# Kernel optimization log

Hardware: AMD Instinct MI355X
Metric: run time of the kernel (lower is better)

Reference implementation:

```python
import jax, jax.numpy as jnp
import numpy as np

K = -1.0          # manifold curvature (hyperbolic / Poincare ball)
SK = 1.0          # sqrt(|K|)
EPS = 1e-7


def _artan_k(x):
    # inverse of tan_k for K<0: artanh(sqrt(|K|) x)/sqrt(|K|)
    return jnp.arctanh(jnp.clip(SK * x, -1.0 + EPS, 1.0 - EPS)) / SK


def _tan_k(x):
    return jnp.tanh(SK * x) / SK


def _norm(x):
    return jnp.maximum(jnp.linalg.norm(x, axis=-1, keepdims=True), 1e-15)


def mobius_add(x, y):
    xy = jnp.sum(x * y, -1, keepdims=True)
    x2 = jnp.sum(x * x, -1, keepdims=True)
    y2 = jnp.sum(y * y, -1, keepdims=True)
    num = (1.0 - 2.0 * K * xy - K * y2) * x + (1.0 + K * x2) * y
    den = 1.0 - 2.0 * K * xy + K * K * x2 * y2
    return num / jnp.maximum(den, 1e-15)


def mobius_scalar_mul(r, x):
    # r may be scalar or (n,1) per-row scalar
    xn = _norm(x)
    return _tan_k(r * _artan_k(xn)) * x / xn


def mobius_matvec(W, x):
    # geoopt convention: (m @ x) per point -> x @ W^T
    xn = _norm(x)
    mx = x @ W.T
    mxn = _norm(mx)
    return _tan_k(mxn / xn * _artan_k(xn)) * mx / mxn


def lambda_x(x):
    # conformal factor lambda_x = 2 / (1 + K |x|^2); returns shape (...,)
    return 2.0 / jnp.maximum(1.0 + K * jnp.sum(x * x, -1), 1e-10)


def expmap0(u):
    un = _norm(u)
    return _tan_k(un) * u / un


def logmap0(y):
    yn = _norm(y)
    return _artan_k(yn) * y / yn


def kappa_left_multiply(A, X):
    # Vectorized per-node weighted gyro-midpoint + mobius scalar mul.
    # out_i = (sum_j A_ij) otimes gyromidpoint(X, weights=A_i)
    gamma = lambda_x(X)                              # (n,)
    denom = A @ (gamma - 1.0)                        # (n,)
    denom = jnp.where(jnp.abs(denom) < 1e-10, 1e-10, denom)
    nom = A @ (gamma[:, None] * X)                   # (n,d)
    two_mean = nom / denom[:, None]
    m = mobius_scalar_mul(0.5, two_mean)             # gyromidpoint
    return mobius_scalar_mul(jnp.sum(A, axis=1, keepdims=True), m)


def setup_inputs() -> dict:
    key = jax.random.key(0)
    k1, k2, k3, k4, k5 = jax.random.split(key, 5)
    n, d, c = 8192, 256, 16
    # node embeddings on the Poincare ball (small norm, well inside the ball)
    X = 0.01 * jax.random.normal(k1, (n, d), jnp.float32)
    # dense normalized adjacency (positive weights, row sums O(1))
    A_hat = jax.random.uniform(k2, (n, n), dtype=jnp.float32) / n
    W = jax.random.uniform(k3, (d, d), dtype=jnp.float32)        # torch.rand init
    W_logits = jax.random.uniform(k4, (d, c), dtype=jnp.float32)
    # p_ks = expmap0(rand), scaled for numerical stability
    p_ks = expmap0(0.05 * jax.random.uniform(k5, (c, d), dtype=jnp.float32))
    return {"X": X, "A_hat": A_hat, "W": W, "W_logits": W_logits, "p_ks": p_ks}


def reference(X, A_hat, W, W_logits, p_ks):
    # hidden kappa-GCN layer
    XW = mobius_matvec(W, X)                          # (n,d)
    AXW = kappa_left_multiply(A_hat, XW)              # (n,d)
    H1 = expmap0(jax.nn.relu(logmap0(AXW)))           # manifold.apply(relu)
    # hyperbolic logits (kappa != 0 branch, K<0 -> asinh)
    z = mobius_add(-p_ks[None, :, :], H1[:, None, :]) # (n,k,d)
    z_n = jnp.linalg.norm(z, axis=-1)                 # (n,k)
    a_n = jnp.maximum(jnp.linalg.norm(W_logits, axis=0), 1e-15)  # (k,)
    za = jnp.einsum('nkd,dk->nk', z, W_logits)
    den = jnp.maximum(1.0 + K * z_n * z_n, 1e-10) * a_n
    dist = jnp.arcsinh(2.0 * SK * za / den)
    lam = lambda_x(p_ks)                              # (k,)
    logits = (lam * a_n / SK) * dist                  # (n,k)
    return A_hat @ logits
```

## Files before the change

kernel.cpp:

```cpp
#include <hip/hip_runtime.h>
#include <math.h>

#define Nn 8192
#define Dd 256
#define Cc 16

#define OFF_BP   4194304u
#define OFF_LOG  5242880u
#define OFF_G1B  5373952u
#define OFF_DEN  5378048u
#define OFF_RS   5410816u
#define OFF_KC   5443584u
#define WS_FLOATS 5443648u

typedef short vshort8 __attribute__((ext_vector_type(8)));
typedef float vfloat4 __attribute__((ext_vector_type(4)));

#define AS1 __attribute__((address_space(1)))
#define AS3 __attribute__((address_space(3)))

__device__ __forceinline__ float clip1(float x) {
    return fminf(fmaxf(x, -1.0f + 1e-7f), 1.0f - 1e-7f);
}

__device__ __forceinline__ unsigned short f2bf(float f) {
    unsigned int u = __float_as_uint(f);
    u += 0x7fff + ((u >> 16) & 1);
    return (unsigned short)(u >> 16);
}

__device__ __forceinline__ float bf2f(unsigned short b) {
    return __uint_as_float(((unsigned int)b) << 16);
}

__device__ __forceinline__ float waveReduce(float v) {
    #pragma unroll
    for (int off = 32; off; off >>= 1) v += __shfl_down(v, off);
    return v;
}

__device__ __forceinline__ float blockReduceBcast(float v, float* red) {
    int t = threadIdx.x, w = t >> 6, l = t & 63;
    v = waveReduce(v);
    if (l == 0) red[w] = v;
    __syncthreads();
    if (t == 0) red[0] = red[0] + red[1] + red[2] + red[3];
    __syncthreads();
    float r = red[0];
    __syncthreads();
    return r;
}

__global__ __launch_bounds__(256) void k_consts(const float* __restrict__ Wl,
                                                const float* __restrict__ Pk,
                                                float* __restrict__ kc) {
    __shared__ float red[8];
    int t = threadIdx.x, k = blockIdx.x;
    float pv = Pk[k * Dd + t];
    float wv = Wl[t * Cc + k];
    float p2 = blockReduceBcast(pv * pv, red);
    float pw = blockReduceBcast(pv * wv, red);
    float w2 = blockReduceBcast(wv * wv, red);
    if (t == 0) {
        float an  = fmaxf(sqrtf(w2), 1e-15f);
        float lam = 2.0f / fmaxf(1.0f - p2, 1e-10f);
        kc[k * 4 + 0] = p2; kc[k * 4 + 1] = pw;
        kc[k * 4 + 2] = an; kc[k * 4 + 3] = lam;
    }
}

__global__ __launch_bounds__(256) void k_front(const float* __restrict__ X,
                                               const float* __restrict__ W,
                                               unsigned short* __restrict__ Bp,
                                               unsigned short* __restrict__ g1b) {
    __shared__ __align__(16) unsigned short Xs[32][256];
    __shared__ __align__(16) unsigned short Gs[32][258];
    __shared__ float xs2[32];
    __shared__ float scal[32];
    __shared__ float red4[32][4];

    const int t = threadIdx.x;
    const int l = t & 63, w = t >> 6;
    const int ll = l & 15, kh = l >> 4;
    const int m0 = blockIdx.x * 32;
    const int ar = t >> 3, aq = t & 7;
    const int c0 = w * 64;

    float x2p = 0.f;
    #pragma unroll
    for (int tc = 0; tc < 4; ++tc) {
        const float* xp = &X[(size_t)(m0 + ar) * Dd + tc * 64 + aq * 8];
        vfloat4 v0 = *(const vfloat4*)xp;
        vfloat4 v1 = *(const vfloat4*)(xp + 4);
        vshort8 o;
        #pragma unroll
        for (int e = 0; e < 4; ++e) {
            x2p += v0[e] * v0[e] + v1[e] * v1[e];
            o[e] = (short)f2bf(v0[e]);
            o[e + 4] = (short)f2bf(v1[e]);
        }
        int byte = (tc * 64 + aq * 8) * 2;
        *(vshort8*)((char*)&Xs[ar][0] + (byte ^ ((ar & 7) << 4))) = o;
    }
    x2p += __shfl_xor(x2p, 1); x2p += __shfl_xor(x2p, 2); x2p += __shfl_xor(x2p, 4);
    if (aq == 0) xs2[ar] = x2p;
    __syncthreads();

    vfloat4 acc[2][4];
    #pragma unroll
    for (int mi = 0; mi < 2; ++mi)
        #pragma unroll
        for (int ni = 0; ni < 4; ++ni)
            acc[mi][ni] = (vfloat4){0.f, 0.f, 0.f, 0.f};
    #pragma unroll
    for (int tc = 0; tc < 4; ++tc) {
        vshort8 bf[8];
        #pragma unroll
        for (int ni = 0; ni < 4; ++ni)
            #pragma unroll
            for (int kk = 0; kk < 2; ++kk) {
                const float* wp = &W[(size_t)(c0 + ni * 16 + ll) * Dd
                                     + tc * 64 + kh * 8 + kk * 32];
                vfloat4 b0 = *(const vfloat4*)wp;
                vfloat4 b1 = *(const vfloat4*)(wp + 4);
                vshort8 o;
                #pragma unroll
                for (int e = 0; e < 4; ++e) {
                    o[e] = (short)f2bf(b0[e]);
                    o[e + 4] = (short)f2bf(b1[e]);
                }
                bf[ni * 2 + kk] = o;
            }
        #pragma unroll
        for (int kk = 0; kk < 2; ++kk) {
            int byte = (tc * 64 + kh * 8 + kk * 32) * 2;
            vshort8 af[2];
            #pragma unroll
            for (int mi = 0; mi < 2; ++mi) {
                int row = mi * 16 + ll;
                af[mi] = *(const vshort8*)((const char*)&Xs[row][0]
                                           + (byte ^ ((row & 7) << 4)));
            }
            #pragma unroll
            for (int mi = 0; mi < 2; ++mi)
                #pragma unroll
                for (int ni = 0; ni < 4; ++ni)
                    acc[mi][ni] = __builtin_amdgcn_mfma_f32_16x16x32_bf16(
                        af[mi], bf[ni * 2 + kk], acc[mi][ni], 0, 0, 0);
        }
    }

    #pragma unroll
    for (int mi = 0; mi < 2; ++mi)
        #pragma unroll
        for (int j = 0; j < 4; ++j) {
            float p = 0.f;
            #pragma unroll
            for (int ni = 0; ni < 4; ++ni)
                p += acc[mi][ni][j] * acc[mi][ni][j];
            p += __shfl_xor(p, 1); p += __shfl_xor(p, 2);
            p += __shfl_xor(p, 4); p += __shfl_xor(p, 8);
            if (ll == 0) red4[mi * 16 + kh * 4 + j][w] = p;
        }
    __syncthreads();

    if (t < 32) {
        float mx2 = red4[t][0] + red4[t][1] + red4[t][2] + red4[t][3];
        float xn = fmaxf(sqrtf(xs2[t]), 1e-15f);
        float mxn = fmaxf(sqrtf(mx2), 1e-15f);
        float s = tanhf(mxn / xn * atanhf(clip1(xn))) / mxn;
        float xw2 = s * s * mx2;
        float gamma = 2.0f / fmaxf(1.0f - xw2, 1e-10f);
        scal[t] = gamma * s;
        g1b[m0 + t] = f2bf(gamma - 1.0f);
    }
    __syncthreads();

    #pragma unroll
    for (int mi = 0; mi < 2; ++mi)
        #pragma unroll
        for (int ni = 0; ni < 4; ++ni) {
            int row = mi * 16 + kh * 4;
            int col = c0 + ni * 16 + ll;
            #pragma unroll
            for (int j = 0; j < 4; ++j)
                Gs[row + j][col] = f2bf(scal[row + j] * acc[mi][ni][j]);
        }
    __syncthreads();

    const int s = blockIdx.x;
    #pragma unroll
    for (int pass = 0; pass < 4; ++pass) {
        int c = pass * 256 + t;
        int gni = c >> 6, lc = c & 63;
        int col = (gni >> 2) * 64 + (gni & 3) * 16 + (lc & 15);
        int kh8 = (lc >> 4) * 8;
        vshort8 o;
        #pragma unroll
        for (int e = 0; e < 8; ++e) o[e] = (short)Gs[kh8 + e][col];
        *(vshort8*)&Bp[((size_t)(s * 16 + gni) * 64 + lc) * 8] = o;
    }
}

__device__ __forceinline__ void g2_issueB(const unsigned short* __restrict__ Bp,
        unsigned short (&BsB)[16][512], int splt, int slab, int w, int l) {
    #pragma unroll
    for (int ni = 0; ni < 4; ++ni)
        __builtin_amdgcn_global_load_lds(
            (const AS1 unsigned int*)
                (Bp + ((size_t)((splt * 64 + slab) * 16 + w * 4 + ni) * 512) + l * 8),
            (AS3 unsigned int*)&BsB[w * 4 + ni][0], 16, 0, 0);
}

__device__ __forceinline__ void g2_loadA(const float* __restrict__ Abase,
                                         int tile, float (&a8)[8]) {
    const vfloat4* p = (const vfloat4*)(Abase + tile * 32);
    *(vfloat4*)&a8[0] = p[0];
    *(vfloat4*)&a8[4] = p[1];
}

__device__ __forceinline__ void g2_stage(unsigned short (&AsB)[2048],
        const unsigned short* g1s, const float (&a8)[8],
        int tile, int rowst, int kq, float& dacc, float& racc) {
    vshort8 gv = *(const vshort8*)&g1s[tile * 32 + kq * 8];
    vshort8 o;
    #pragma unroll
    for (int e = 0; e < 8; ++e) {
        float av = a8[e];
        o[e] = (short)f2bf(av);
        dacc += av * bf2f((unsigned short)gv[e]);
        racc += av;
    }
    *(vshort8*)((char*)&AsB[0] + rowst * 64 + ((kq * 16) ^ ((rowst & 3) << 4))) = o;
}

__device__ __forceinline__ void g2_mfma(const unsigned short (&AsB)[2048],
        const unsigned short (&BsB)[16][512], int w, int kh, int ll15, int l,
        vfloat4 (&acc)[4][4]) {
    vshort8 bf[4], af[4];
    #pragma unroll
    for (int ni = 0; ni < 4; ++ni)
        bf[ni] = *(const vshort8*)&BsB[w * 4 + ni][l * 8];
    #pragma unroll
    for (int mi = 0; mi < 4; ++mi) {
        int row = mi * 16 + ll15;
        af[mi] = *(const vshort8*)((const char*)&AsB[0]
                  + row * 64 + ((kh * 16) ^ ((row & 3) << 4)));
    }
    __builtin_amdgcn_s_setprio(1);
    #pragma unroll
    for (int mi = 0; mi < 4; ++mi)
        #pragma unroll
        for (int ni = 0; ni < 4; ++ni)
            acc[mi][ni] = __builtin_amdgcn_mfma_f32_16x16x32_bf16(
                af[mi], bf[ni], acc[mi][ni], 0, 0, 0);
    __builtin_amdgcn_s_setprio(0);
}

__global__ __launch_bounds__(256, 2) void k_gemm1_mfma(
        const float* __restrict__ A,
        const unsigned short* __restrict__ Bp,
        const unsigned short* __restrict__ g1b,
        unsigned short* __restrict__ Pp,
        float* __restrict__ denp,
        float* __restrict__ rsp) {
    __shared__ __align__(16) unsigned short As[2][2048];
    __shared__ __align__(16) unsigned short Bs[4][16][512];
    __shared__ __align__(16) unsigned short g1s[2048];

    const int t = threadIdx.x, l = t & 63, w = t >> 6;
    const int id = blockIdx.x;
    const int splt = id & 3;
    const int m0 = (id >> 2) * 64;
    const int kb = splt * 2048;
    const int kh = l >> 4, ll15 = l & 15;
    const int rowst = t >> 2, kq = t & 3;

    const float* Abase = &A[(size_t)(m0 + rowst) * Nn + kb + kq * 8];

    vfloat4 acc[4][4];
    #pragma unroll
    for (int mi = 0; mi < 4; ++mi)
        #pragma unroll
        for (int ni = 0; ni < 4; ++ni)
            acc[mi][ni] = (vfloat4){0.f, 0.f, 0.f, 0.f};
    float dacc = 0.f, racc = 0.f;
    float a0[8], a1[8], a2[8], a3[8];

    uint4 g1v = *(const uint4*)&g1b[kb + t * 8];
    g2_issueB(Bp, Bs[0], splt, 0, w, l);
    g2_issueB(Bp, Bs[1], splt, 1, w, l);
    g2_issueB(Bp, Bs[2], splt, 2, w, l);
    g2_loadA(Abase, 0, a0);
    g2_loadA(Abase, 1, a1);
    g2_loadA(Abase, 2, a2);
    g2_loadA(Abase, 3, a3);
    asm volatile("s_waitcnt vmcnt(0)" ::: "memory");
    *(uint4*)&g1s[t * 8] = g1v;
    asm volatile("s_waitcnt lgkmcnt(0)" ::: "memory");
    __builtin_amdgcn_s_barrier();
    g2_stage(As[0], g1s, a0, 0, rowst, kq, dacc, racc);
    asm volatile("s_waitcnt lgkmcnt(0)" ::: "memory");
    __builtin_amdgcn_s_barrier();
    __builtin_amdgcn_sched_barrier(0);

    for (int u = 0; u < 16; ++u) {
        #pragma unroll
        for (int pp = 0; pp < 4; ++pp) {
            const int q = u * 4 + pp;
            g2_issueB(Bp, Bs[(pp + 3) & 3], splt, (q + 3) & 63, w, l);
            {
                float (&adst)[8] = (pp == 0) ? a0 : (pp == 1) ? a1
                                 : (pp == 2) ? a2 : a3;
                g2_loadA(Abase, (q + 4) & 63, adst);
            }
            asm volatile("s_waitcnt vmcnt(18)" ::: "memory");
            if (q < 63) {
                float (&asrc)[8] = (pp == 0) ? a1 : (pp == 1) ? a2
                                 : (pp == 2) ? a3 : a0;
                g2_stage(As[(q + 1) & 1], g1s, asrc, q + 1, rowst, kq, dacc, racc);
            }
            g2_mfma(As[q & 1], Bs[pp & 3], w, kh, ll15, l, acc);
            asm volatile("s_waitcnt lgkmcnt(0)" ::: "memory");
            __builtin_amdgcn_s_barrier();
            __builtin_amdgcn_sched_barrier(0);
        }
    }

    dacc += __shfl_xor(dacc, 1); dacc += __shfl_xor(dacc, 2);
    racc += __shfl_xor(racc, 1); racc += __shfl_xor(racc, 2);
    if (kq == 0) {
        denp[splt * Nn + m0 + rowst] = dacc;
        rsp [splt * Nn + m0 + rowst] = racc;
    }

    unsigned short* P = Pp + (size_t)splt * ((size_t)Nn * Dd);
    #pragma unroll
    for (int mi = 0; mi < 4; ++mi)
        #pragma unroll
        for (int ni = 0; ni < 4; ++ni) {
            int row = m0 + mi * 16 + (kh << 2);
            int col = w * 64 + ni * 16 + ll15;
            #pragma unroll
            for (int j = 0; j < 4; ++j)
                P[(size_t)(row + j) * Dd + col] = f2bf(acc[mi][ni][j]);
        }
}

__global__ __launch_bounds__(256) void k_rowfix(const unsigned short* __restrict__ Pp,
                                                const float* __restrict__ denp,
                                                const float* __restrict__ rsp,
                                                const float* __restrict__ Pk,
                                                const float* __restrict__ Wl,
                                                const float* __restrict__ kc,
                                                float* __restrict__ logits) {
    __shared__ float red[8];
    __shared__ float hs[256];
    __shared__ float PQ[16][2];
    int i = blockIdx.x, t = threadIdx.x;
    float nom = 0.f;
    #pragma unroll
    for (int s = 0; s < 4; ++s)
        nom += bf2f(Pp[(size_t)s * Nn * Dd + (size_t)i * Dd + t]);
    float dv = denp[i] + denp[Nn + i] + denp[2 * Nn + i] + denp[3 * Nn + i];
    dv = (fabsf(dv) < 1e-10f) ? 1e-10f : dv;
    float tm = nom / dv;
    float r2 = blockReduceBcast(tm * tm, red);
    float r = fmaxf(sqrtf(r2), 1e-15f);
    float mmul = tanhf(0.5f * atanhf(clip1(r))) / r;
    float mj = mmul * tm;
    float mn2 = blockReduceBcast(mj * mj, red);
    float mn = fmaxf(sqrtf(mn2), 1e-15f);
    float sA = rsp[i] + rsp[Nn + i] + rsp[2 * Nn + i] + rsp[3 * Nn + i];
    float axmul = tanhf(sA * atanhf(clip1(mn))) / mn;
    float axw = axmul * mj;
    float yn2 = blockReduceBcast(axw * axw, red);
    float yn = fmaxf(sqrtf(yn2), 1e-15f);
    float v = atanhf(clip1(yn)) / yn * axw;
    float u = fmaxf(v, 0.0f);
    float un2 = blockReduceBcast(u * u, red);
    float un = fmaxf(sqrtf(un2), 1e-15f);
    float h = tanhf(un) / un * u;
    float h2 = blockReduceBcast(h * h, red);
    hs[t] = h;
    __syncthreads();
    int w = t >> 6, l = t & 63;
    #pragma unroll
    for (int kk = 0; kk < 4; ++kk) {
        int k = w * 4 + kk;
        float pp = 0.f, qq = 0.f;
        #pragma unroll
        for (int m = 0; m < 4; ++m) {
            float hv = hs[l + 64 * m];
            pp += hv * Pk[k * Dd + l + 64 * m];
            qq += hv * Wl[(l + 64 * m) * Cc + k];
        }
        pp = waveReduce(pp);
        qq = waveReduce(qq);
        if (l == 0) { PQ[k][0] = pp; PQ[k][1] = qq; }
    }
    __syncthreads();
    if (t < 16) {
        int k = t;
        float p2 = kc[k * 4 + 0], pw = kc[k * 4 + 1];
        float an = kc[k * 4 + 2], lam = kc[k * 4 + 3];
        float P = PQ[k][0], Q = PQ[k][1];
        float alpha = 1.0f - 2.0f * P + h2;
        float beta  = 1.0f - p2;
        float Dm = fmaxf(1.0f - 2.0f * P + p2 * h2, 1e-15f);
        float za  = (-alpha * pw + beta * Q) / Dm;
        float zn2 = (alpha * alpha * p2 - 2.0f * alpha * beta * P + beta * beta * h2)
                    / (Dm * Dm);
        float dd = fmaxf(1.0f - zn2, 1e-10f) * an;
        float dist = asinhf(2.0f * za / dd);
        logits[(size_t)i * Cc + k] = lam * an * dist;
    }
}

__global__ __launch_bounds__(256) void k_gemm2(const float* __restrict__ A,
                                               const float* __restrict__ L,
                                               float* __restrict__ part) {
    __shared__ __align__(16) float Ls[64 * 20];
    __shared__ float Pacc[256 * 16];
    int t = threadIdx.x;
    int r0 = blockIdx.x * 256;
    int jbase = blockIdx.y * 512;
    int q = t & 3, g = t >> 2;
    float acc[4][16] = {};
    for (int jc = 0; jc < 512; jc += 64) {
        {
            int jrow = t >> 2, kq2 = t & 3;
            *(float4*)&Ls[jrow * 20 + kq2 * 4] =
                *(const float4*)&L[(size_t)(jbase + jc + jrow) * Cc + kq2 * 4];
        }
        __syncthreads();
        #pragma unroll
        for (int m = 0; m < 4; ++m) {
            int jl = m * 16 + q * 4;
            float av[4][4];
            #pragma unroll
            for (int rr = 0; rr < 4; ++rr) {
                float4 tmp = *(const float4*)&A[(size_t)(r0 + g * 4 + rr) * Nn
                                                + jbase + jc + jl];
                av[rr][0] = tmp.x; av[rr][1] = tmp.y;
                av[rr][2] = tmp.z; av[rr][3] = tmp.w;
            }
            #pragma unroll
            for (int jj = 0; jj < 4; ++jj) {
                const float* lr = &Ls[(jl + jj) * 20];
                float lv[16];
                #pragma unroll
                for (int k2 = 0; k2 < 16; k2 += 4) {
                    float4 lt = *(const float4*)&lr[k2];
                    lv[k2] = lt.x; lv[k2 + 1] = lt.y;
                    lv[k2 + 2] = lt.z; lv[k2 + 3] = lt.w;
                }
                #pragma unroll
                for (int rr = 0; rr < 4; ++rr)
                    #pragma unroll
                    for (int k2 = 0; k2 < 16; ++k2)
                        acc[rr][k2] += av[rr][jj] * lv[k2];
            }
        }
        __syncthreads();
    }
    for (int ii = t; ii < 4096; ii += 256) Pacc[ii] = 0.f;
    __syncthreads();
    for (int qq = 0; qq < 4; ++qq) {
        if (q == qq) {
            #pragma unroll
            for (int rr = 0; rr < 4; ++rr)
                #pragma unroll
                for (int k2 = 0; k2 < 16; ++k2)
                    Pacc[(g * 4 + rr) * 16 + k2] += acc[rr][k2];
        }
        __syncthreads();
    }
    float* dst = &part[(size_t)blockIdx.y * (Nn * Cc) + (size_t)r0 * Cc];
    for (int ii = t * 4; ii < 4096; ii += 1024)
        *(float4*)&dst[ii] = *(const float4*)&Pacc[ii];
}

__global__ __launch_bounds__(256) void k_reduce(const float* __restrict__ part,
                                                float* __restrict__ out) {
    int i = blockIdx.x * 256 + threadIdx.x;
    float s = 0.f;
    #pragma unroll
    for (int j = 0; j < 16; ++j) s += part[(size_t)j * (Nn * Cc) + i];
    out[i] = s;
}

extern "C" void kernel_launch(void* const* d_in, const int* in_sizes, int n_in,
                              void* d_out, int out_size, void* d_ws, size_t ws_size,
                              hipStream_t stream) {
    const float* X  = (const float*)d_in[0];
    const float* A  = (const float*)d_in[1];
    const float* W  = (const float*)d_in[2];
    const float* Wl = (const float*)d_in[3];
    const float* Pk = (const float*)d_in[4];
    float* out = (float*)d_out;
    float* ws = (float*)d_ws;
    if (ws_size < (size_t)WS_FLOATS * sizeof(float)) return;

    unsigned short* Pp  = (unsigned short*)ws;
    float* part = ws;
    unsigned short* Bp  = (unsigned short*)(ws + OFF_BP);
    float* lg   = ws + OFF_LOG;
    unsigned short* g1b = (unsigned short*)(ws + OFF_G1B);
    float* denp = ws + OFF_DEN;
    float* rsp  = ws + OFF_RS;
    float* kc   = ws + OFF_KC;

    k_consts<<<16, 256, 0, stream>>>(Wl, Pk, kc);
    k_front<<<256, 256, 0, stream>>>(X, W, Bp, g1b);
    k_gemm1_mfma<<<512, 256, 0, stream>>>(A, Bp, g1b, Pp, denp, rsp);
    k_rowfix<<<Nn, 256, 0, stream>>>(Pp, denp, rsp, Pk, Wl, kc, lg);
    k_gemm2<<<dim3(32, 16), 256, 0, stream>>>(A, lg, part);
    k_reduce<<<512, 256, 0, stream>>>(part, out);
}
```

Measured before the change: 212.8 us.

## Restage A@logits GEMM through LDS with direct global-to-LDS loads and swizzle

Rewrites the second GEMM (A_hat @ logits) so each block loads a 64x256 tile of A and the matching logits rows straight into LDS with global_load_lds, using an XOR swizzle to avoid bank conflicts. Each thread keeps one row's 16 accumulators and walks a quarter of the K range, and a small LDS reduction replaces the serialized Pacc accumulation loop. The grid changes from 32x16 to 128x8 blocks, so the split-K reduce sums 8 partials instead of 16. The intent is coalesced, asynchronous loading of the 256 MB A read and less reduction traffic. In exchange there is no double buffering: loads and compute are serialized within each tile, and LDS use per block grows.

After: 298.0 us. 1.4x slower.

```diff
diff --git a/kernel.cpp b/kernel.cpp
--- a/kernel.cpp
+++ b/kernel.cpp
@@ -417,68 +417,68 @@
     }
 }
 
-__global__ __launch_bounds__(256) void k_gemm2(const float* __restrict__ A,
-                                               const float* __restrict__ L,
-                                               float* __restrict__ part) {
-    __shared__ __align__(16) float Ls[64 * 20];
-    __shared__ float Pacc[256 * 16];
-    int t = threadIdx.x;
-    int r0 = blockIdx.x * 256;
-    int jbase = blockIdx.y * 512;
-    int q = t & 3, g = t >> 2;
-    float acc[4][16] = {};
-    for (int jc = 0; jc < 512; jc += 64) {
-        {
-            int jrow = t >> 2, kq2 = t & 3;
-            *(float4*)&Ls[jrow * 20 + kq2 * 4] =
-                *(const float4*)&L[(size_t)(jbase + jc + jrow) * Cc + kq2 * 4];
-        }
-        __syncthreads();
-        #pragma unroll
-        for (int m = 0; m < 4; ++m) {
-            int jl = m * 16 + q * 4;
-            float av[4][4];
-            #pragma unroll
-            for (int rr = 0; rr < 4; ++rr) {
-                float4 tmp = *(const float4*)&A[(size_t)(r0 + g * 4 + rr) * Nn
-                                                + jbase + jc + jl];
-                av[rr][0] = tmp.x; av[rr][1] = tmp.y;
-                av[rr][2] = tmp.z; av[rr][3] = tmp.w;
+__global__ __launch_bounds__(256, 2) void k_gemm2(const float* __restrict__ A,
+                                                  const float* __restrict__ L,
+                                                  float* __restrict__ part) {
+    __shared__ __align__(16) float Al[64 * 256];
+    __shared__ __align__(16) float Ls[256 * 16];
+    const int t = threadIdx.x, l = t & 63, w = t >> 6;
+    const int m0 = blockIdx.x * 64;
+    const int jb = blockIdx.y;
+    const int g = t >> 2, q = t & 3;
+    float acc[16] = {};
+
+    for (int tile = 0; tile < 4; ++tile) {
+        int jc = jb * 1024 + tile * 256;
+        #pragma unroll
+        for (int rr = 0; rr < 16; ++rr) {
+            int row = rr * 4 + w;
+            const float* src = &A[(size_t)(m0 + row) * Nn + jc
+                                  + ((l * 4) ^ ((row & 7) * 4))];
+            __builtin_amdgcn_global_load_lds((const AS1 unsigned int*)src,
+                (AS3 unsigned int*)&Al[row * 256], 16, 0, 0);
+        }
+        #pragma unroll
+        for (int i = 0; i < 4; ++i) {
+            int chunk = i * 4 + w;
+            const float* src = &L[(size_t)jc * Cc + chunk * 256 + l * 4];
+            __builtin_amdgcn_global_load_lds((const AS1 unsigned int*)src,
+                (AS3 unsigned int*)&Ls[chunk * 256], 16, 0, 0);
+        }
+        asm volatile("s_waitcnt vmcnt(0)" ::: "memory");
+        __builtin_amdgcn_s_barrier();
+
+        for (int jj4 = 0; jj4 < 16; ++jj4) {
+            int jl = q * 64 + jj4 * 4;
+            vfloat4 av = *(const vfloat4*)&Al[g * 256 + (jl ^ ((g & 7) * 4))];
+            #pragma unroll
+            for (int e = 0; e < 4; ++e) {
+                const float* lr = &Ls[(jl + e) * 16];
+                #pragma unroll
+                for (int k4 = 0; k4 < 4; ++k4) {
+                    vfloat4 lv = *(const vfloat4*)&lr[k4 * 4];
+                    #pragma unroll
+                    for (int kk = 0; kk < 4; ++kk)
+                        acc[k4 * 4 + kk] += av[e] * lv[kk];
+                }
             }
-            #pragma unroll
-            for (int jj = 0; jj < 4; ++jj) {
-                const float* lr = &Ls[(jl + jj) * 20];
-                float lv[16];
-                #pragma unroll
-                for (int k2 = 0; k2 < 16; k2 += 4) {
-                    float4 lt = *(const float4*)&lr[k2];
-                    lv[k2] = lt.x; lv[k2 + 1] = lt.y;
-                    lv[k2 + 2] = lt.z; lv[k2 + 3] = lt.w;
-                }
-                #pragma unroll
-                for (int rr = 0; rr < 4; ++rr)
-                    #pragma unroll
-                    for (int k2 = 0; k2 < 16; ++k2)
-                        acc[rr][k2] += av[rr][jj] * lv[k2];
-            }
-        }
-        __syncthreads();
-    }
-    for (int ii = t; ii < 4096; ii += 256) Pacc[ii] = 0.f;
-    __syncthreads();
-    for (int qq = 0; qq < 4; ++qq) {
-        if (q == qq) {
-            #pragma unroll
-            for (int rr = 0; rr < 4; ++rr)
-                #pragma unroll
-                for (int k2 = 0; k2 < 16; ++k2)
-                    Pacc[(g * 4 + rr) * 16 + k2] += acc[rr][k2];
-        }
-        __syncthreads();
-    }
-    float* dst = &part[(size_t)blockIdx.y * (Nn * Cc) + (size_t)r0 * Cc];
-    for (int ii = t * 4; ii < 4096; ii += 1024)
-        *(float4*)&dst[ii] = *(const float4*)&Pacc[ii];
+        }
+        __builtin_amdgcn_s_barrier();
+    }
+
+    #pragma unroll
+    for (int k4 = 0; k4 < 4; ++k4)
+        *(vfloat4*)&Al[(g * 4 + q) * 16 + k4 * 4] =
+            (vfloat4){acc[k4 * 4], acc[k4 * 4 + 1], acc[k4 * 4 + 2], acc[k4 * 4 + 3]};
+    __syncthreads();
+    #pragma unroll
+    for (int pass = 0; pass < 4; ++pass) {
+        int idx = pass * 256 + t;
+        int row = idx >> 4, k = idx & 15;
+        float s = Al[(row * 4 + 0) * 16 + k] + Al[(row * 4 + 1) * 16 + k]
+                + Al[(row * 4 + 2) * 16 + k] + Al[(row * 4 + 3) * 16 + k];
+        part[((size_t)jb * Nn + m0 + row) * Cc + k] = s;
+    }
 }
 
 __global__ __launch_bounds__(256) void k_reduce(const float* __restrict__ part,
@@ -486,7 +486,7 @@
     int i = blockIdx.x * 256 + threadIdx.x;
     float s = 0.f;
     #pragma unroll
-    for (int j = 0; j < 16; ++j) s += part[(size_t)j * (Nn * Cc) + i];
+    for (int j = 0; j < 8; ++j) s += part[(size_t)j * (Nn * Cc) + i];
     out[i] = s;
 }
 
@@ -515,6 +515,6 @@
     k_front<<<256, 256, 0, stream>>>(X, W, Bp, g1b);
     k_gemm1_mfma<<<512, 256, 0, stream>>>(A, Bp, g1b, Pp, denp, rsp);
     k_rowfix<<<Nn, 256, 0, stream>>>(Pp, denp, rsp, Pk, Wl, kc, lg);
-    k_gemm2<<<dim3(32, 16), 256, 0, stream>>>(A, lg, part);
+    k_gemm2<<<dim3(128, 8), 256, 0, stream>>>(A, lg, part);
     k_reduce<<<512, 256, 0, stream>>>(part, out);
 }
```
